# Optimization experiments

Measured on AMD Instinct MI355X. Metric: run time of the kernel, lower is better.

The kernel has to match this reference:

```python
import jax, jax.numpy as jnp
import numpy as np

N_NODES = 16384
N_EDGES = 524288
IN_CH = 128
HID_CH = 128
N_CLUST = 128


def _gcn_conv(x, W, b, src, dst, n):
    """PyG GCNConv: out = D^{-1/2} (A + I) D^{-1/2} (x @ W) + b, aggregating src -> dst."""
    h = x @ W  # [N, out]
    loop = jnp.arange(n)
    row = jnp.concatenate([src, loop])  # message sources (incl. self loops)
    col = jnp.concatenate([dst, loop])  # message targets
    deg = jax.ops.segment_sum(jnp.ones(row.shape, dtype=h.dtype), col, num_segments=n)
    dinv = jax.lax.rsqrt(deg)  # deg >= 1 thanks to self loops
    w = dinv[row] * dinv[col]  # [E + N]
    out = jax.ops.segment_sum(h[row] * w[:, None], col, num_segments=n)
    return out + b


def setup_inputs() -> dict:
    key = jax.random.key(0)
    k1, k2, k3, k4 = jax.random.split(key, 4)
    x = jax.random.normal(k1, (N_NODES, IN_CH), dtype=jnp.float32)
    edge_index = jax.random.randint(k2, (2, N_EDGES), 0, N_NODES, dtype=jnp.int64)
    W_emb = jax.random.normal(k3, (IN_CH, HID_CH), dtype=jnp.float32) / np.sqrt(IN_CH)
    b_emb = jnp.zeros((HID_CH,), dtype=jnp.float32)
    W_asn = jax.random.normal(k4, (IN_CH, N_CLUST), dtype=jnp.float32) / np.sqrt(IN_CH)
    b_asn = jnp.zeros((N_CLUST,), dtype=jnp.float32)
    return {"x": x, "edge_index": edge_index, "W_emb": W_emb, "b_emb": b_emb,
            "W_asn": W_asn, "b_asn": b_asn}


def reference(x, edge_index, W_emb, b_emb, W_asn, b_asn):
    n = x.shape[0]
    src, dst = edge_index[0], edge_index[1]
    x_emb = jax.nn.relu(_gcn_conv(x, W_emb, b_emb, src, dst, n))        # [N, H]
    S = jax.nn.softmax(_gcn_conv(x, W_asn, b_asn, src, dst, n), axis=-1)  # [N, K]
    x_pooled = S.T @ x_emb                                               # [K, H]
    A = jnp.zeros((n, n), dtype=x.dtype).at[src, dst].set(1.0)           # dense adjacency
    A_pooled = (S.T @ A) @ S                                             # [K, K]
    # torch code returns A_pooled.nonzero().T (dynamic shape, not jit-able);
    # we return the dense pooled adjacency carrying the same information.
    return x_pooled, A_pooled, S
```

## Files before the change

### kernel.cpp

```cpp
#include <hip/hip_runtime.h>

#define N_NODES 16384
#define N_EDGES 524288

typedef short bf16x8 __attribute__((ext_vector_type(8)));
typedef float f32x4 __attribute__((ext_vector_type(4)));

__device__ __forceinline__ ushort f2bf(float a) {
    uint u = __float_as_uint(a);
    return (ushort)((u + 0x7fff + ((u >> 16) & 1)) >> 16);
}
__device__ __forceinline__ uint pack2bf(float a, float b) {
    return (uint)f2bf(a) | ((uint)f2bf(b) << 16);
}
__device__ __forceinline__ float bflo(uint v) { return __uint_as_float(v << 16); }
__device__ __forceinline__ float bfhi(uint v) { return __uint_as_float(v & 0xffff0000u); }

__global__ void prep_kernel(uint4* __restrict__ count4, const float* __restrict__ W_emb,
                            const float* __restrict__ W_asn, ushort* __restrict__ wT) {
    int b = blockIdx.x;
    if (b < 16) { count4[b * 256 + threadIdx.x] = make_uint4(0, 0, 0, 0); return; }
    int idx = (b - 16) * 256 + threadIdx.x;
    int k = idx >> 8, n = idx & 255;
    float v = n < 128 ? W_emb[k * 128 + n] : W_asn[k * 128 + (n - 128)];
    wT[(size_t)n * 128 + k] = f2bf(v);
}

__global__ void hist_kernel(const int* __restrict__ dst, int* __restrict__ count) {
    int e = blockIdx.x * 256 + threadIdx.x;
    if (e < N_EDGES) atomicAdd(&count[dst[e]], 1);
}

__global__ __launch_bounds__(256) void scan_kernel(
        const int* __restrict__ count, int* __restrict__ indptr,
        int* __restrict__ cursor, float* __restrict__ dinv) {
    __shared__ int lds[64 * 257];
    __shared__ int part[256];
    int t = threadIdx.x;
#pragma unroll 4
    for (int j = 0; j < 64; ++j) {
        int e = j * 256 + t;
        lds[(e & 63) * 257 + (e >> 6)] = count[e];
    }
    __syncthreads();
    int s = 0;
#pragma unroll
    for (int i = 0; i < 64; ++i) {
        int idx = i * 257 + t;
        int v = lds[idx];
        lds[idx] = s;
        s += v;
    }
    part[t] = s;
    __syncthreads();
    for (int off = 1; off < 256; off <<= 1) {
        int v = (t >= off) ? part[t - off] : 0;
        __syncthreads();
        part[t] += v;
        __syncthreads();
    }
    int prefix = (t == 0) ? 0 : part[t - 1];
#pragma unroll
    for (int i = 0; i < 64; ++i) lds[i * 257 + t] += prefix;
    __syncthreads();
#pragma unroll 4
    for (int j = 0; j < 64; ++j) {
        int e = j * 256 + t;
        int p = lds[(e & 63) * 257 + (e >> 6)];
        indptr[e] = p;
        cursor[e] = p;
        dinv[e] = rsqrtf((float)(count[e] + 1));
    }
    if (t == 0) indptr[N_NODES] = N_EDGES;
}

__global__ void scatter_cvt_kernel(const int* __restrict__ src, const int* __restrict__ dst,
                                   int* __restrict__ cursor, int* __restrict__ sorted_src,
                                   const float* __restrict__ x, const float* __restrict__ dinv,
                                   ushort* __restrict__ x_bf) {
    int b = blockIdx.x;
    if (b < 2048) {
        int e = b * 256 + threadIdx.x;
        int d = dst[e];
        int p = atomicAdd(&cursor[d], 1);
        sorted_src[p] = src[e];
    } else {
        int i = (b - 2048) * 256 + threadIdx.x;
        float4 v = *(const float4*)(x + (size_t)i * 4);
        float dv = dinv[i >> 5];
        ushort4 o;
        o.x = f2bf(v.x * dv); o.y = f2bf(v.y * dv);
        o.z = f2bf(v.z * dv); o.w = f2bf(v.w * dv);
        *(ushort4*)(x_bf + (size_t)i * 4) = o;
    }
}

__global__ void agg_kernel(const uint2* __restrict__ xp2, const int* __restrict__ indptr,
                           const int* __restrict__ sorted_src, const float* __restrict__ dinv,
                           uint2* __restrict__ agg2) {
    int wv = threadIdx.x >> 6, lane = threadIdx.x & 63;
    int d = blockIdx.x * 4 + wv;
    int beg = indptr[d], end = indptr[d + 1];
    int half = lane >> 5, hl = lane & 31;
    float a0 = 0.f, a1 = 0.f, a2 = 0.f, a3 = 0.f;
    for (int ch = beg; ch < end; ch += 64) {
        int take = end - ch; if (take > 64) take = 64;
        int myi = sorted_src[ch + (lane < take ? lane : 0)];
        int i = 0;
        for (; i + 8 <= take; i += 8) {
            int s0 = __shfl(myi, i + half);
            int s1 = __shfl(myi, i + 2 + half);
            int s2 = __shfl(myi, i + 4 + half);
            int s3 = __shfl(myi, i + 6 + half);
            uint2 v0 = xp2[(size_t)s0 * 32 + hl];
            uint2 v1 = xp2[(size_t)s1 * 32 + hl];
            uint2 v2 = xp2[(size_t)s2 * 32 + hl];
            uint2 v3 = xp2[(size_t)s3 * 32 + hl];
            a0 += (bflo(v0.x) + bflo(v1.x)) + (bflo(v2.x) + bflo(v3.x));
            a1 += (bfhi(v0.x) + bfhi(v1.x)) + (bfhi(v2.x) + bfhi(v3.x));
            a2 += (bflo(v0.y) + bflo(v1.y)) + (bflo(v2.y) + bflo(v3.y));
            a3 += (bfhi(v0.y) + bfhi(v1.y)) + (bfhi(v2.y) + bfhi(v3.y));
        }
        for (; i + 2 <= take; i += 2) {
            int s = __shfl(myi, i + half);
            uint2 v = xp2[(size_t)s * 32 + hl];
            a0 += bflo(v.x); a1 += bfhi(v.x); a2 += bflo(v.y); a3 += bfhi(v.y);
        }
        if (i < take) {
            int s = __shfl(myi, i);
            if (half == 0) {
                uint2 v = xp2[(size_t)s * 32 + hl];
                a0 += bflo(v.x); a1 += bfhi(v.x); a2 += bflo(v.y); a3 += bfhi(v.y);
            }
        }
    }
    a0 += __shfl_xor(a0, 32); a1 += __shfl_xor(a1, 32);
    a2 += __shfl_xor(a2, 32); a3 += __shfl_xor(a3, 32);
    if (half == 0) {
        uint2 vd = xp2[(size_t)d * 32 + hl];
        a0 += bflo(vd.x); a1 += bfhi(vd.x); a2 += bflo(vd.y); a3 += bfhi(vd.y);
        float di = dinv[d];
        uint2 o; o.x = pack2bf(a0 * di, a1 * di); o.y = pack2bf(a2 * di, a3 * di);
        agg2[(size_t)d * 32 + hl] = o;
    }
}

__global__ __launch_bounds__(512) void gemm_fused_mfma(
        const ushort* __restrict__ agg, const ushort* __restrict__ wT,
        const float* __restrict__ b_emb, const float* __restrict__ b_asn,
        float* __restrict__ S_out, uint* __restrict__ S_bf,
        ushort* __restrict__ xe_T, ushort* __restrict__ S_T) {
    __shared__ float hs[64][257];
    int l = threadIdx.x & 63, w = threadIdx.x >> 6;
    int lrow0 = (w >> 2) * 32;
    int m0 = blockIdx.x * 64 + lrow0;
    int n0 = (w & 3) * 64;
    int lr = l & 15, lk = (l >> 4) * 8;
    f32x4 acc[2][4] = {};
#pragma unroll
    for (int kk = 0; kk < 128; kk += 32) {
        bf16x8 a[2], b[4];
#pragma unroll
        for (int fm = 0; fm < 2; ++fm)
            a[fm] = *(const bf16x8*)(agg + (size_t)(m0 + fm * 16 + lr) * 128 + kk + lk);
#pragma unroll
        for (int fn = 0; fn < 4; ++fn)
            b[fn] = *(const bf16x8*)(wT + (size_t)(n0 + fn * 16 + lr) * 128 + kk + lk);
#pragma unroll
        for (int fm = 0; fm < 2; ++fm)
#pragma unroll
            for (int fn = 0; fn < 4; ++fn)
                acc[fm][fn] = __builtin_amdgcn_mfma_f32_16x16x32_bf16(
                    a[fm], b[fn], acc[fm][fn], 0, 0, 0);
    }
    int rbase = (l >> 4) * 4;
    const float* __restrict__ bvec = n0 < 128 ? b_emb : b_asn;
    int bcol0 = n0 & 127;
#pragma unroll
    for (int fn = 0; fn < 4; ++fn) {
        float bias = bvec[bcol0 + fn * 16 + lr];
#pragma unroll
        for (int fm = 0; fm < 2; ++fm)
#pragma unroll
            for (int r = 0; r < 4; ++r)
                hs[lrow0 + fm * 16 + rbase + r][n0 + fn * 16 + lr] = acc[fm][fn][r] + bias;
    }
    __syncthreads();
    int g = threadIdx.x >> 3, sub = threadIdx.x & 7;
    size_t grow = blockIdx.x * 64 + g;
#pragma unroll
    for (int j = 0; j < 16; ++j) {
        float a0 = fmaxf(hs[g][sub * 16 + j], 0.f);
        hs[g][sub * 16 + j] = a0;
    }
    float v[16];
#pragma unroll
    for (int j = 0; j < 16; ++j) v[j] = hs[g][128 + sub * 16 + j];
    float m = v[0];
#pragma unroll
    for (int j = 1; j < 16; ++j) m = fmaxf(m, v[j]);
    m = fmaxf(m, __shfl_xor(m, 1));
    m = fmaxf(m, __shfl_xor(m, 2));
    m = fmaxf(m, __shfl_xor(m, 4));
    float s = 0.f;
#pragma unroll
    for (int j = 0; j < 16; ++j) { v[j] = __expf(v[j] - m); s += v[j]; }
    s += __shfl_xor(s, 1);
    s += __shfl_xor(s, 2);
    s += __shfl_xor(s, 4);
    float inv = 1.f / s;
    uint w8[8];
#pragma unroll
    for (int j = 0; j < 16; ++j) { v[j] *= inv; hs[g][128 + sub * 16 + j] = v[j]; }
#pragma unroll
    for (int q = 0; q < 4; ++q)
        *(float4*)(&S_out[grow * 128 + sub * 16 + 4 * q]) =
            make_float4(v[4 * q], v[4 * q + 1], v[4 * q + 2], v[4 * q + 3]);
#pragma unroll
    for (int j = 0; j < 8; ++j) w8[j] = pack2bf(v[2 * j], v[2 * j + 1]);
    *(uint4*)(&S_bf[grow * 64 + sub * 8])     = make_uint4(w8[0], w8[1], w8[2], w8[3]);
    *(uint4*)(&S_bf[grow * 64 + sub * 8 + 4]) = make_uint4(w8[4], w8[5], w8[6], w8[7]);
    __syncthreads();
    int brow = blockIdx.x * 64;
#pragma unroll
    for (int r = 0; r < 4; ++r) {
        int c = (threadIdx.x >> 3) + 64 * r;
        int oct = threadIdx.x & 7;
        uint w4[4];
#pragma unroll
        for (int q = 0; q < 4; ++q) {
            float u0 = hs[oct * 8 + 2 * q][c];
            float u1 = hs[oct * 8 + 2 * q + 1][c];
            w4[q] = pack2bf(u0, u1);
        }
        ushort* __restrict__ T = c < 128 ? xe_T : S_T;
        *(uint4*)(&T[(size_t)(c & 127) * N_NODES + brow + oct * 8]) =
            make_uint4(w4[0], w4[1], w4[2], w4[3]);
    }
}

__global__ void mt_kernel(const uint2* __restrict__ Sp2, const int* __restrict__ indptr,
                          const int* __restrict__ sorted_src, uint2* __restrict__ Mt2) {
    int wv = threadIdx.x >> 6, lane = threadIdx.x & 63;
    int d = blockIdx.x * 4 + wv;
    int beg = indptr[d], end = indptr[d + 1];
    int half = lane >> 5, hl = lane & 31;
    float a0 = 0.f, a1 = 0.f, a2 = 0.f, a3 = 0.f;
    for (int ch = beg; ch < end; ch += 64) {
        int take = end - ch; if (take > 64) take = 64;
        int myv = sorted_src[ch + (lane < take ? lane : 0)];
        bool dup = false;
        for (int r = 1; r < 64; ++r) {
            int ov = __shfl(myv, (lane - r) & 63);
            if (lane >= r && lane < take && ov == myv) dup = true;
        }
        for (int pc = beg; pc < ch; pc += 64) {
            int ov = sorted_src[pc + lane];
            for (int r = 0; r < 64; ++r) {
                int u = __shfl(ov, r);
                if (lane < take && u == myv) dup = true;
            }
        }
        int fl = myv | (dup ? (int)0x80000000 : 0);
        int i = 0;
        for (; i + 8 <= take; i += 8) {
            int s0 = __shfl(fl, i + half);
            int s1 = __shfl(fl, i + 2 + half);
            int s2 = __shfl(fl, i + 4 + half);
            int s3 = __shfl(fl, i + 6 + half);
            float m0 = s0 >= 0 ? 1.f : 0.f, m1 = s1 >= 0 ? 1.f : 0.f;
            float m2 = s2 >= 0 ? 1.f : 0.f, m3 = s3 >= 0 ? 1.f : 0.f;
            uint2 v0 = Sp2[(size_t)(s0 & 16383) * 32 + hl];
            uint2 v1 = Sp2[(size_t)(s1 & 16383) * 32 + hl];
            uint2 v2 = Sp2[(size_t)(s2 & 16383) * 32 + hl];
            uint2 v3 = Sp2[(size_t)(s3 & 16383) * 32 + hl];
            a0 += (bflo(v0.x) * m0 + bflo(v1.x) * m1) + (bflo(v2.x) * m2 + bflo(v3.x) * m3);
            a1 += (bfhi(v0.x) * m0 + bfhi(v1.x) * m1) + (bfhi(v2.x) * m2 + bfhi(v3.x) * m3);
            a2 += (bflo(v0.y) * m0 + bflo(v1.y) * m1) + (bflo(v2.y) * m2 + bflo(v3.y) * m3);
            a3 += (bfhi(v0.y) * m0 + bfhi(v1.y) * m1) + (bfhi(v2.y) * m2 + bfhi(v3.y) * m3);
        }
        for (; i + 2 <= take; i += 2) {
            int s = __shfl(fl, i + half);
            if (s >= 0) {
                uint2 v = Sp2[(size_t)(s & 16383) * 32 + hl];
                a0 += bflo(v.x); a1 += bfhi(v.x); a2 += bflo(v.y); a3 += bfhi(v.y);
            }
        }
        if (i < take) {
            int s = __shfl(fl, i);
            if (half == 0 && s >= 0) {
                uint2 v = Sp2[(size_t)(s & 16383) * 32 + hl];
                a0 += bflo(v.x); a1 += bfhi(v.x); a2 += bflo(v.y); a3 += bfhi(v.y);
            }
        }
    }
    a0 += __shfl_xor(a0, 32); a1 += __shfl_xor(a1, 32);
    a2 += __shfl_xor(a2, 32); a3 += __shfl_xor(a3, 32);
    if (half == 0) {
        uint2 o; o.x = pack2bf(a0, a1); o.y = pack2bf(a2, a3);
        Mt2[(size_t)d * 32 + hl] = o;
    }
}

__global__ __launch_bounds__(256) void transpose_kernel(
        const ushort* __restrict__ Mt_bf, ushort* __restrict__ Mt_T) {
    __shared__ ushort tile[128][130];
    int tid = threadIdx.x;
    int n0 = blockIdx.x * 128;
    for (int i = tid; i < 2048; i += 256) {
        int r = i >> 4, c8 = (i & 15) << 3;
        const uint* p = (const uint*)(Mt_bf + (size_t)(n0 + r) * 128 + c8);
        uint* t = (uint*)&tile[r][c8];
        t[0] = p[0]; t[1] = p[1]; t[2] = p[2]; t[3] = p[3];
    }
    __syncthreads();
    for (int i = tid; i < 2048; i += 256) {
        int ch = i >> 4, n8 = (i & 15) << 3;
        ushort v[8];
#pragma unroll
        for (int j = 0; j < 8; ++j) v[j] = tile[n8 + j][ch];
        uint4 o;
        o.x = (uint)v[0] | ((uint)v[1] << 16);
        o.y = (uint)v[2] | ((uint)v[3] << 16);
        o.z = (uint)v[4] | ((uint)v[5] << 16);
        o.w = (uint)v[6] | ((uint)v[7] << 16);
        *(uint4*)(Mt_T + (size_t)ch * N_NODES + n0 + n8) = o;
    }
}

__global__ __launch_bounds__(512) void pool_stage1_mfma(
        const ushort* __restrict__ S_T, const ushort* __restrict__ xe_T,
        const ushort* __restrict__ Mt_T, float* __restrict__ part) {
    const ushort* __restrict__ A = blockIdx.y ? Mt_T : S_T;
    const ushort* __restrict__ B = blockIdx.y ? S_T : xe_T;
    float* __restrict__ out = part + (size_t)blockIdx.y * (128 * 16384) +
                              (size_t)blockIdx.x * 16384;
    int l = threadIdx.x & 63, w = threadIdx.x >> 6;
    int m0 = (w >> 2) * 64;
    int n0 = (w & 3) * 32;
    int lr = l & 15, lk = (l >> 4) * 8;
    int kb = blockIdx.x * 128;
    f32x4 acc[4][2] = {};
#pragma unroll
    for (int kk = 0; kk < 128; kk += 32) {
        bf16x8 a[4], b[2];
#pragma unroll
        for (int fm = 0; fm < 4; ++fm)
            a[fm] = *(const bf16x8*)(A + (size_t)(m0 + fm * 16 + lr) * N_NODES + kb + kk + lk);
#pragma unroll
        for (int fn = 0; fn < 2; ++fn)
            b[fn] = *(const bf16x8*)(B + (size_t)(n0 + fn * 16 + lr) * N_NODES + kb + kk + lk);
#pragma unroll
        for (int fm = 0; fm < 4; ++fm)
#pragma unroll
            for (int fn = 0; fn < 2; ++fn)
                acc[fm][fn] = __builtin_amdgcn_mfma_f32_16x16x32_bf16(
                    a[fm], b[fn], acc[fm][fn], 0, 0, 0);
    }
    int rbase = (l >> 4) * 4;
#pragma unroll
    for (int fm = 0; fm < 4; ++fm)
#pragma unroll
        for (int r = 0; r < 4; ++r)
#pragma unroll
            for (int fn = 0; fn < 2; ++fn)
                out[(size_t)(m0 + fm * 16 + rbase + r) * 128 + n0 + fn * 16 + lr] =
                    acc[fm][fn][r];
}

__global__ void pool_reduce_kernel(const float* __restrict__ part, float* __restrict__ out) {
    int idx = blockIdx.x * 256 + threadIdx.x;
    int g = idx >> 14;
    int o = idx & 16383;
    const float* __restrict__ p = part + (size_t)g * (128 * 16384) + o;
    float s = 0.f;
#pragma unroll 8
    for (int c = 0; c < 128; ++c) s += p[(size_t)c * 16384];
    out[idx] = s;
}

extern "C" void kernel_launch(void* const* d_in, const int* in_sizes, int n_in,
                              void* d_out, int out_size, void* d_ws, size_t ws_size,
                              hipStream_t stream) {
    const float* x      = (const float*)d_in[0];
    const int*   ei     = (const int*)d_in[1];
    const float* W_emb  = (const float*)d_in[2];
    const float* b_emb  = (const float*)d_in[3];
    const float* W_asn  = (const float*)d_in[4];
    const float* b_asn  = (const float*)d_in[5];
    const int* src = ei;
    const int* dst = ei + N_EDGES;

    float* out = (float*)d_out;
    float* S_out = out + 32768;

    char* ws = (char*)d_ws;
    ushort* x_bf    = (ushort*)(ws + 0);
    ushort* S_T     = (ushort*)(ws + 0);
    ushort* agg     = (ushort*)(ws + 4194304);
    ushort* Mt_T    = (ushort*)(ws + 4194304);
    ushort* xe_T    = (ushort*)(ws + 8388608);
    int*    sorted  = (int*)   (ws + 12582912);
    ushort* wT      = (ushort*)(ws + 14680064);
    int*    count   = (int*)   (ws + 15204352);
    int*    indptr  = (int*)   (ws + 15269888);
    int*    cursor  = (int*)   (ws + 15400960);
    float*  dinv    = (float*) (ws + 15466496);
    uint*   S_bf    = (uint*)  (ws + 16777216);
    uint*   Mt_bf   = (uint*)  (ws + 20971520);
    float*  part    = (float*) (ws + 16777216);

    prep_kernel<<<144, 256, 0, stream>>>((uint4*)count, W_emb, W_asn, wT);
    hist_kernel<<<2048, 256, 0, stream>>>(dst, count);
    scan_kernel<<<1, 256, 0, stream>>>(count, indptr, cursor, dinv);
    scatter_cvt_kernel<<<4096, 256, 0, stream>>>(src, dst, cursor, sorted, x, dinv, x_bf);
    agg_kernel<<<4096, 256, 0, stream>>>((const uint2*)x_bf, indptr, sorted, dinv,
                                         (uint2*)agg);
    gemm_fused_mfma<<<256, 512, 0, stream>>>(agg, wT, b_emb, b_asn, S_out, S_bf, xe_T, S_T);
    mt_kernel<<<4096, 256, 0, stream>>>((const uint2*)S_bf, indptr, sorted, (uint2*)Mt_bf);
    transpose_kernel<<<128, 256, 0, stream>>>((const ushort*)Mt_bf, Mt_T);
    pool_stage1_mfma<<<dim3(128, 2), 512, 0, stream>>>(S_T, xe_T, Mt_T, part);
    pool_reduce_kernel<<<128, 256, 0, stream>>>(part, out);
}
```

Measured before the change: 145.7 us.

## Fuse Mt transpose into pooling GEMM via LDS and widen scan to 1024 threads

Drops the separate transpose kernel. The pooling GEMM now loads row-major Mt chunks into shared memory and transposes them there before the MFMA. Each block also covers twice the K range, which halves the number of partial sums the reduce kernel has to add. The single-block scan now uses 1024 threads with wave shuffle prefix sums in place of the barrier-heavy LDS Hillis-Steele scan. In exchange, the y=1 blocks take extra barriers and strided LDS writes that may bank-conflict, and only 128 GEMM blocks are launched, which lowers parallelism.

```diff
diff --git a/kernel.cpp b/kernel.cpp
--- a/kernel.cpp
+++ b/kernel.cpp
@@ -31,42 +31,52 @@
     if (e < N_EDGES) atomicAdd(&count[dst[e]], 1);
 }
 
-__global__ __launch_bounds__(256) void scan_kernel(
+__global__ __launch_bounds__(1024) void scan_kernel(
         const int* __restrict__ count, int* __restrict__ indptr,
         int* __restrict__ cursor, float* __restrict__ dinv) {
-    __shared__ int lds[64 * 257];
-    __shared__ int part[256];
+    __shared__ int lds[16 * 1041];
+    __shared__ int wsum[16];
     int t = threadIdx.x;
-#pragma unroll 4
-    for (int j = 0; j < 64; ++j) {
-        int e = j * 256 + t;
-        lds[(e & 63) * 257 + (e >> 6)] = count[e];
+#pragma unroll
+    for (int j = 0; j < 16; ++j) {
+        int e = j * 1024 + t;
+        lds[(t & 15) * 1041 + j * 64 + (t >> 4)] = count[e];
     }
     __syncthreads();
     int s = 0;
 #pragma unroll
-    for (int i = 0; i < 64; ++i) {
-        int idx = i * 257 + t;
+    for (int i = 0; i < 16; ++i) {
+        int idx = i * 1041 + t;
         int v = lds[idx];
         lds[idx] = s;
         s += v;
     }
-    part[t] = s;
-    __syncthreads();
-    for (int off = 1; off < 256; off <<= 1) {
-        int v = (t >= off) ? part[t - off] : 0;
-        __syncthreads();
-        part[t] += v;
-        __syncthreads();
-    }
-    int prefix = (t == 0) ? 0 : part[t - 1];
-#pragma unroll
-    for (int i = 0; i < 64; ++i) lds[i * 257 + t] += prefix;
-    __syncthreads();
-#pragma unroll 4
-    for (int j = 0; j < 64; ++j) {
-        int e = j * 256 + t;
-        int p = lds[(e & 63) * 257 + (e >> 6)];
+    int lane = t & 63, wid = t >> 6;
+    int incl = s;
+    for (int d = 1; d < 64; d <<= 1) {
+        int tmp = __shfl_up(incl, d);
+        if (lane >= d) incl += tmp;
+    }
+    if (lane == 63) wsum[wid] = incl;
+    __syncthreads();
+    if (wid == 0) {
+        int v = (lane < 16) ? wsum[lane] : 0;
+        int ic = v;
+        for (int d = 1; d < 16; d <<= 1) {
+            int tmp = __shfl_up(ic, d);
+            if (lane >= d) ic += tmp;
+        }
+        if (lane < 16) wsum[lane] = ic - v;
+    }
+    __syncthreads();
+    int base = wsum[wid] + (incl - s);
+#pragma unroll
+    for (int i = 0; i < 16; ++i) lds[i * 1041 + t] += base;
+    __syncthreads();
+#pragma unroll
+    for (int j = 0; j < 16; ++j) {
+        int e = j * 1024 + t;
+        int p = lds[(t & 15) * 1041 + j * 64 + (t >> 4)];
         indptr[e] = p;
         cursor[e] = p;
         dinv[e] = rsqrtf((float)(count[e] + 1));
@@ -302,60 +312,57 @@
     }
 }
 
-__global__ __launch_bounds__(256) void transpose_kernel(
-        const ushort* __restrict__ Mt_bf, ushort* __restrict__ Mt_T) {
-    __shared__ ushort tile[128][130];
-    int tid = threadIdx.x;
-    int n0 = blockIdx.x * 128;
-    for (int i = tid; i < 2048; i += 256) {
-        int r = i >> 4, c8 = (i & 15) << 3;
-        const uint* p = (const uint*)(Mt_bf + (size_t)(n0 + r) * 128 + c8);
-        uint* t = (uint*)&tile[r][c8];
-        t[0] = p[0]; t[1] = p[1]; t[2] = p[2]; t[3] = p[3];
-    }
-    __syncthreads();
-    for (int i = tid; i < 2048; i += 256) {
-        int ch = i >> 4, n8 = (i & 15) << 3;
-        ushort v[8];
-#pragma unroll
-        for (int j = 0; j < 8; ++j) v[j] = tile[n8 + j][ch];
-        uint4 o;
-        o.x = (uint)v[0] | ((uint)v[1] << 16);
-        o.y = (uint)v[2] | ((uint)v[3] << 16);
-        o.z = (uint)v[4] | ((uint)v[5] << 16);
-        o.w = (uint)v[6] | ((uint)v[7] << 16);
-        *(uint4*)(Mt_T + (size_t)ch * N_NODES + n0 + n8) = o;
-    }
-}
-
 __global__ __launch_bounds__(512) void pool_stage1_mfma(
         const ushort* __restrict__ S_T, const ushort* __restrict__ xe_T,
-        const ushort* __restrict__ Mt_T, float* __restrict__ part) {
-    const ushort* __restrict__ A = blockIdx.y ? Mt_T : S_T;
-    const ushort* __restrict__ B = blockIdx.y ? S_T : xe_T;
-    float* __restrict__ out = part + (size_t)blockIdx.y * (128 * 16384) +
-                              (size_t)blockIdx.x * 16384;
+        const ushort* __restrict__ Mt_bf, float* __restrict__ part0,
+        float* __restrict__ part1) {
+    __shared__ ushort tile[128][136];
     int l = threadIdx.x & 63, w = threadIdx.x >> 6;
     int m0 = (w >> 2) * 64;
     int n0 = (w & 3) * 32;
     int lr = l & 15, lk = (l >> 4) * 8;
-    int kb = blockIdx.x * 128;
+    int y = blockIdx.y;
+    const ushort* __restrict__ B = y ? S_T : xe_T;
+    float* __restrict__ out = (y ? part1 : part0) + (size_t)blockIdx.x * 16384;
     f32x4 acc[4][2] = {};
-#pragma unroll
-    for (int kk = 0; kk < 128; kk += 32) {
-        bf16x8 a[4], b[2];
-#pragma unroll
-        for (int fm = 0; fm < 4; ++fm)
-            a[fm] = *(const bf16x8*)(A + (size_t)(m0 + fm * 16 + lr) * N_NODES + kb + kk + lk);
-#pragma unroll
-        for (int fn = 0; fn < 2; ++fn)
-            b[fn] = *(const bf16x8*)(B + (size_t)(n0 + fn * 16 + lr) * N_NODES + kb + kk + lk);
-#pragma unroll
-        for (int fm = 0; fm < 4; ++fm)
+    for (int kb2 = 0; kb2 < 2; ++kb2) {
+        int kb = blockIdx.x * 256 + kb2 * 128;
+        if (y) {
+            __syncthreads();
+            for (int cc = threadIdx.x; cc < 2048; cc += 512) {
+                int row = cc >> 4;
+                int c8 = (cc & 15) << 3;
+                uint4 v = *(const uint4*)(Mt_bf + (size_t)(kb + row) * 128 + c8);
+                ushort* pv = (ushort*)&v;
+#pragma unroll
+                for (int j = 0; j < 8; ++j) tile[c8 + j][row] = pv[j];
+            }
+            __syncthreads();
+        }
+#pragma unroll
+        for (int kk = 0; kk < 128; kk += 32) {
+            bf16x8 a[4], b[2];
+            if (y) {
+#pragma unroll
+                for (int fm = 0; fm < 4; ++fm)
+                    a[fm] = *(const bf16x8*)&tile[m0 + fm * 16 + lr][kk + lk];
+            } else {
+#pragma unroll
+                for (int fm = 0; fm < 4; ++fm)
+                    a[fm] = *(const bf16x8*)(S_T + (size_t)(m0 + fm * 16 + lr) * N_NODES
+                                             + kb + kk + lk);
+            }
 #pragma unroll
             for (int fn = 0; fn < 2; ++fn)
-                acc[fm][fn] = __builtin_amdgcn_mfma_f32_16x16x32_bf16(
-                    a[fm], b[fn], acc[fm][fn], 0, 0, 0);
+                b[fn] = *(const bf16x8*)(B + (size_t)(n0 + fn * 16 + lr) * N_NODES
+                                         + kb + kk + lk);
+#pragma unroll
+            for (int fm = 0; fm < 4; ++fm)
+#pragma unroll
+                for (int fn = 0; fn < 2; ++fn)
+                    acc[fm][fn] = __builtin_amdgcn_mfma_f32_16x16x32_bf16(
+                        a[fm], b[fn], acc[fm][fn], 0, 0, 0);
+        }
     }
     int rbase = (l >> 4) * 4;
 #pragma unroll
@@ -368,14 +375,14 @@
                     acc[fm][fn][r];
 }
 
-__global__ void pool_reduce_kernel(const float* __restrict__ part, float* __restrict__ out) {
+__global__ void pool_reduce_kernel(const float* __restrict__ part0,
+                                   const float* __restrict__ part1,
+                                   float* __restrict__ out) {
     int idx = blockIdx.x * 256 + threadIdx.x;
-    int g = idx >> 14;
-    int o = idx & 16383;
-    const float* __restrict__ p = part + (size_t)g * (128 * 16384) + o;
+    const float* __restrict__ p = (idx < 16384 ? part0 : part1) + (idx & 16383);
     float s = 0.f;
 #pragma unroll 8
-    for (int c = 0; c < 128; ++c) s += p[(size_t)c * 16384];
+    for (int c = 0; c < 64; ++c) s += p[(size_t)c * 16384];
     out[idx] = s;
 }
 
@@ -398,7 +405,7 @@
     ushort* x_bf    = (ushort*)(ws + 0);
     ushort* S_T     = (ushort*)(ws + 0);
     ushort* agg     = (ushort*)(ws + 4194304);
-    ushort* Mt_T    = (ushort*)(ws + 4194304);
+    float*  part0   = (float*) (ws + 4194304);
     ushort* xe_T    = (ushort*)(ws + 8388608);
     int*    sorted  = (int*)   (ws + 12582912);
     ushort* wT      = (ushort*)(ws + 14680064);
@@ -407,18 +414,18 @@
     int*    cursor  = (int*)   (ws + 15400960);
     float*  dinv    = (float*) (ws + 15466496);
     uint*   S_bf    = (uint*)  (ws + 16777216);
+    float*  part1   = (float*) (ws + 16777216);
     uint*   Mt_bf   = (uint*)  (ws + 20971520);
-    float*  part    = (float*) (ws + 16777216);
 
     prep_kernel<<<144, 256, 0, stream>>>((uint4*)count, W_emb, W_asn, wT);
     hist_kernel<<<2048, 256, 0, stream>>>(dst, count);
-    scan_kernel<<<1, 256, 0, stream>>>(count, indptr, cursor, dinv);
+    scan_kernel<<<1, 1024, 0, stream>>>(count, indptr, cursor, dinv);
     scatter_cvt_kernel<<<4096, 256, 0, stream>>>(src, dst, cursor, sorted, x, dinv, x_bf);
     agg_kernel<<<4096, 256, 0, stream>>>((const uint2*)x_bf, indptr, sorted, dinv,
                                          (uint2*)agg);
     gemm_fused_mfma<<<256, 512, 0, stream>>>(agg, wT, b_emb, b_asn, S_out, S_bf, xe_T, S_T);
     mt_kernel<<<4096, 256, 0, stream>>>((const uint2*)S_bf, indptr, sorted, (uint2*)Mt_bf);
-    transpose_kernel<<<128, 256, 0, stream>>>((const ushort*)Mt_bf, Mt_T);
-    pool_stage1_mfma<<<dim3(128, 2), 512, 0, stream>>>(S_T, xe_T, Mt_T, part);
-    pool_reduce_kernel<<<128, 256, 0, stream>>>(part, out);
-}
+    pool_stage1_mfma<<<dim3(64, 2), 512, 0, stream>>>(S_T, xe_T, (const ushort*)Mt_bf,
+                                                      part0, part1);
+    pool_reduce_kernel<<<128, 256, 0, stream>>>(part0, part1, out);
+}
```

After: 140.7 us (median of 2 runs). -3.4%, faster.
